# Optimization experiments

Hardware: AMD Instinct MI355X
Metric: run time of the kernel (lower is better)

Reference implementation:

```python
import jax, jax.numpy as jnp
import numpy as np

N_CLASS = 4432          # 1108 siRNA classes x 4 cell types
N_GROUPS = 4
GROUP_SIZE = N_CLASS // N_GROUPS  # 1108
LABEL_SMOOTHING = 0.1
CONFIDENCE = 1.0 - LABEL_SMOOTHING
SMOOTHING_VALUE = LABEL_SMOOTHING / (GROUP_SIZE - 1)


def setup_inputs() -> dict:
    key = jax.random.key(0)
    k1, k2 = jax.random.split(key)
    output = jax.random.normal(k1, (16384, N_CLASS), dtype=jnp.float32)
    target = jax.random.randint(k2, (16384,), 0, N_CLASS, dtype=jnp.int64)
    return {"output": output, "target": target}


def reference(output, target):
    # output: [B, C] logits, target: [B] int labels
    log_output = jax.nn.log_softmax(output, axis=1)                      # [B, C]
    classes = jnp.arange(N_CLASS, dtype=target.dtype)                    # [C]
    one_hot = jnp.where(classes[None, :] == target[:, None],
                        CONFIDENCE, SMOOTHING_VALUE).astype(output.dtype)  # [B, C]
    # group of each class (4 cell-type groups, contiguous blocks of GROUP_SIZE)
    class_group = classes // GROUP_SIZE                                  # [C]
    target_group = target // GROUP_SIZE                                  # [B]
    # zero smoothed mass for classes outside the sample's group (masks[group])
    one_hot = jnp.where(class_group[None, :] == target_group[:, None], one_hot, 0.0)
    loss = -(one_hot * log_output).sum(axis=1)                           # [B]
    return jnp.mean(loss)
```

## Files before the change

### kernel.cpp

```cpp
#include <hip/hip_runtime.h>
#include <math.h>

#define N_CLASS   4432
#define GROUP_SZ  1108
#define NV4       (N_CLASS / 4)
#define GV4       (GROUP_SZ / 4)
#define NROWS     16384
#define BLOCK     256

static constexpr float CONF   = 0.9f;
static constexpr float SMOOTH = 0.1f / (GROUP_SZ - 1);

template <bool WS_MODE>
__global__ __launch_bounds__(BLOCK)
void lsl_kernel(const float* __restrict__ logits,
                const int*   __restrict__ target,
                float*       __restrict__ sink) {
    const int row = blockIdx.x;
    const float4* __restrict__ rp = (const float4*)(logits + (size_t)row * N_CLASS);

    const int t      = target[row];
    const int g      = t / GROUP_SZ;
    const int glo    = g * GV4;
    const int ghi    = glo + GV4;
    const int tchunk = t >> 2;
    const int tlane  = t & 3;
    const int tid    = threadIdx.x;

    const int  c4    = tid + 1024;
    const bool have5 = (c4 < NV4);

    float4 v0 = rp[tid];
    float4 v1 = rp[tid + 256];
    float4 v2 = rp[tid + 512];
    float4 v3 = rp[tid + 768];
    float4 v4 = make_float4(-INFINITY, -INFINITY, -INFINITY, -INFINITY);
    if (have5) v4 = rp[c4];

    float m = fmaxf(fmaxf(fmaxf(v0.x, v0.y), fmaxf(v0.z, v0.w)),
                    fmaxf(fmaxf(v1.x, v1.y), fmaxf(v1.z, v1.w)));
    m = fmaxf(m, fmaxf(fmaxf(v2.x, v2.y), fmaxf(v2.z, v2.w)));
    m = fmaxf(m, fmaxf(fmaxf(v3.x, v3.y), fmaxf(v3.z, v3.w)));
    m = fmaxf(m, fmaxf(fmaxf(v4.x, v4.y), fmaxf(v4.z, v4.w)));

    #pragma unroll
    for (int off = 32; off > 0; off >>= 1)
        m = fmaxf(m, __shfl_xor(m, off));

    __shared__ float m_s[4], s_s[4], g_s[4];
    __shared__ float xt_s;
    const int wave = tid >> 6;
    const int lane = tid & 63;
    if (lane == 0) m_s[wave] = m;
    __syncthreads();
    const float M = fmaxf(fmaxf(m_s[0], m_s[1]), fmaxf(m_s[2], m_s[3]));

    float s = __expf(v0.x - M) + __expf(v0.y - M) + __expf(v0.z - M) + __expf(v0.w - M)
            + __expf(v1.x - M) + __expf(v1.y - M) + __expf(v1.z - M) + __expf(v1.w - M)
            + __expf(v2.x - M) + __expf(v2.y - M) + __expf(v2.z - M) + __expf(v2.w - M)
            + __expf(v3.x - M) + __expf(v3.y - M) + __expf(v3.z - M) + __expf(v3.w - M)
            + __expf(v4.x - M) + __expf(v4.y - M) + __expf(v4.z - M) + __expf(v4.w - M);

    float gsum = 0.f;
    {
        int c0 = tid;
        if (c0 >= glo && c0 < ghi) gsum += (v0.x + v0.y) + (v0.z + v0.w);
        int c1 = tid + 256;
        if (c1 >= glo && c1 < ghi) gsum += (v1.x + v1.y) + (v1.z + v1.w);
        int c2 = tid + 512;
        if (c2 >= glo && c2 < ghi) gsum += (v2.x + v2.y) + (v2.z + v2.w);
        int c3 = tid + 768;
        if (c3 >= glo && c3 < ghi) gsum += (v3.x + v3.y) + (v3.z + v3.w);
        if (have5 && c4 >= glo && c4 < ghi) gsum += (v4.x + v4.y) + (v4.z + v4.w);
    }

    {
        float4 tv; bool has_t = false;
        if (tid == tchunk)              { tv = v0; has_t = true; }
        else if (tid + 256 == tchunk)   { tv = v1; has_t = true; }
        else if (tid + 512 == tchunk)   { tv = v2; has_t = true; }
        else if (tid + 768 == tchunk)   { tv = v3; has_t = true; }
        else if (have5 && c4 == tchunk) { tv = v4; has_t = true; }
        if (has_t) {
            xt_s = (tlane == 0) ? tv.x : (tlane == 1) ? tv.y
                 : (tlane == 2) ? tv.z : tv.w;
        }
    }

    #pragma unroll
    for (int off = 32; off > 0; off >>= 1) {
        s    += __shfl_xor(s, off);
        gsum += __shfl_xor(gsum, off);
    }
    if (lane == 0) { s_s[wave] = s; g_s[wave] = gsum; }
    __syncthreads();

    if (tid == 0) {
        float S = (s_s[0] + s_s[1]) + (s_s[2] + s_s[3]);
        float G = (g_s[0] + g_s[1]) + (g_s[2] + g_s[3]);
        float lse  = M + __logf(S);
        float loss = lse - ((CONF - SMOOTH) * xt_s + SMOOTH * G);
        if (WS_MODE) sink[row] = loss;
        else         atomicAdd(sink, loss * (1.0f / NROWS));
    }
}

__global__ __launch_bounds__(256)
void lsl_reduce(const float* __restrict__ ws, float* __restrict__ out) {
    const float4* wp = (const float4*)ws;
    const int tid = threadIdx.x;
    float s = 0.f;
    #pragma unroll
    for (int i = 0; i < NROWS / 4 / 256; ++i) {
        float4 v = wp[tid + i * 256];
        s += (v.x + v.y) + (v.z + v.w);
    }
    #pragma unroll
    for (int off = 32; off > 0; off >>= 1) s += __shfl_xor(s, off);
    __shared__ float ss[4];
    const int wave = tid >> 6, lane = tid & 63;
    if (lane == 0) ss[wave] = s;
    __syncthreads();
    if (tid == 0) out[0] = ((ss[0] + ss[1]) + (ss[2] + ss[3])) * (1.0f / NROWS);
}

extern "C" void kernel_launch(void* const* d_in, const int* in_sizes, int n_in,
                              void* d_out, int out_size, void* d_ws, size_t ws_size,
                              hipStream_t stream) {
    const float* logits = (const float*)d_in[0];
    const int*   target = (const int*)d_in[1];
    float*       result = (float*)d_out;
    float*       ws     = (float*)d_ws;

    if (ws_size >= (size_t)NROWS * sizeof(float)) {
        lsl_kernel<true><<<NROWS, BLOCK, 0, stream>>>(logits, target, ws);
        lsl_reduce<<<1, 256, 0, stream>>>(ws, result);
    } else {
        hipMemsetAsync(result, 0, sizeof(float), stream);
        lsl_kernel<false><<<NROWS, BLOCK, 0, stream>>>(logits, target, result);
    }
}
```

Baseline: 381.9 us.

## Assign one wavefront per row and drop block-level syncs

Each 256-thread block now handles four rows, one per wavefront. Each lane loads 18 float4 chunks and all reductions (max, sum-exp, group sum, target logit) use wave shuffles only. This removes the shared-memory exchanges and the two __syncthreads per row, and gives each wave more outstanding loads. The cost is a larger register array per thread, which may reduce occupancy.

```diff
diff --git a/kernel.cpp b/kernel.cpp
--- a/kernel.cpp
+++ b/kernel.cpp
@@ -7,6 +7,9 @@
 #define GV4       (GROUP_SZ / 4)
 #define NROWS     16384
 #define BLOCK     256
+#define FULL_IT   17
+#define TAIL_BASE (FULL_IT * 64)
+#define TAIL_N    (NV4 - TAIL_BASE)
 
 static constexpr float CONF   = 0.9f;
 static constexpr float SMOOTH = 0.1f / (GROUP_SZ - 1);
@@ -16,7 +19,9 @@
 void lsl_kernel(const float* __restrict__ logits,
                 const int*   __restrict__ target,
                 float*       __restrict__ sink) {
-    const int row = blockIdx.x;
+    const int wave = threadIdx.x >> 6;
+    const int lane = threadIdx.x & 63;
+    const int row  = blockIdx.x * 4 + wave;
     const float4* __restrict__ rp = (const float4*)(logits + (size_t)row * N_CLASS);
 
     const int t      = target[row];
@@ -25,81 +30,50 @@
     const int ghi    = glo + GV4;
     const int tchunk = t >> 2;
     const int tlane  = t & 3;
-    const int tid    = threadIdx.x;
 
-    const int  c4    = tid + 1024;
-    const bool have5 = (c4 < NV4);
+    float4 v[FULL_IT + 1];
+    #pragma unroll
+    for (int i = 0; i < FULL_IT; ++i) v[i] = rp[lane + 64 * i];
+    const bool have18 = (lane < TAIL_N);
+    v[FULL_IT] = make_float4(-INFINITY, -INFINITY, -INFINITY, -INFINITY);
+    if (have18) v[FULL_IT] = rp[TAIL_BASE + lane];
 
-    float4 v0 = rp[tid];
-    float4 v1 = rp[tid + 256];
-    float4 v2 = rp[tid + 512];
-    float4 v3 = rp[tid + 768];
-    float4 v4 = make_float4(-INFINITY, -INFINITY, -INFINITY, -INFINITY);
-    if (have5) v4 = rp[c4];
-
-    float m = fmaxf(fmaxf(fmaxf(v0.x, v0.y), fmaxf(v0.z, v0.w)),
-                    fmaxf(fmaxf(v1.x, v1.y), fmaxf(v1.z, v1.w)));
-    m = fmaxf(m, fmaxf(fmaxf(v2.x, v2.y), fmaxf(v2.z, v2.w)));
-    m = fmaxf(m, fmaxf(fmaxf(v3.x, v3.y), fmaxf(v3.z, v3.w)));
-    m = fmaxf(m, fmaxf(fmaxf(v4.x, v4.y), fmaxf(v4.z, v4.w)));
-
+    float m = -INFINITY;
+    #pragma unroll
+    for (int i = 0; i <= FULL_IT; ++i)
+        m = fmaxf(m, fmaxf(fmaxf(v[i].x, v[i].y), fmaxf(v[i].z, v[i].w)));
     #pragma unroll
     for (int off = 32; off > 0; off >>= 1)
         m = fmaxf(m, __shfl_xor(m, off));
 
-    __shared__ float m_s[4], s_s[4], g_s[4];
-    __shared__ float xt_s;
-    const int wave = tid >> 6;
-    const int lane = tid & 63;
-    if (lane == 0) m_s[wave] = m;
-    __syncthreads();
-    const float M = fmaxf(fmaxf(m_s[0], m_s[1]), fmaxf(m_s[2], m_s[3]));
-
-    float s = __expf(v0.x - M) + __expf(v0.y - M) + __expf(v0.z - M) + __expf(v0.w - M)
-            + __expf(v1.x - M) + __expf(v1.y - M) + __expf(v1.z - M) + __expf(v1.w - M)
-            + __expf(v2.x - M) + __expf(v2.y - M) + __expf(v2.z - M) + __expf(v2.w - M)
-            + __expf(v3.x - M) + __expf(v3.y - M) + __expf(v3.z - M) + __expf(v3.w - M)
-            + __expf(v4.x - M) + __expf(v4.y - M) + __expf(v4.z - M) + __expf(v4.w - M);
-
-    float gsum = 0.f;
-    {
-        int c0 = tid;
-        if (c0 >= glo && c0 < ghi) gsum += (v0.x + v0.y) + (v0.z + v0.w);
-        int c1 = tid + 256;
-        if (c1 >= glo && c1 < ghi) gsum += (v1.x + v1.y) + (v1.z + v1.w);
-        int c2 = tid + 512;
-        if (c2 >= glo && c2 < ghi) gsum += (v2.x + v2.y) + (v2.z + v2.w);
-        int c3 = tid + 768;
-        if (c3 >= glo && c3 < ghi) gsum += (v3.x + v3.y) + (v3.z + v3.w);
-        if (have5 && c4 >= glo && c4 < ghi) gsum += (v4.x + v4.y) + (v4.z + v4.w);
+    float s = 0.f;
+    #pragma unroll
+    for (int i = 0; i <= FULL_IT; ++i) {
+        s += __expf(v[i].x - m) + __expf(v[i].y - m)
+           + __expf(v[i].z - m) + __expf(v[i].w - m);
     }
 
-    {
-        float4 tv; bool has_t = false;
-        if (tid == tchunk)              { tv = v0; has_t = true; }
-        else if (tid + 256 == tchunk)   { tv = v1; has_t = true; }
-        else if (tid + 512 == tchunk)   { tv = v2; has_t = true; }
-        else if (tid + 768 == tchunk)   { tv = v3; has_t = true; }
-        else if (have5 && c4 == tchunk) { tv = v4; has_t = true; }
-        if (has_t) {
-            xt_s = (tlane == 0) ? tv.x : (tlane == 1) ? tv.y
-                 : (tlane == 2) ? tv.z : tv.w;
-        }
+    float gsum = 0.f, xt = 0.f;
+    #pragma unroll
+    for (int i = 0; i <= FULL_IT; ++i) {
+        const int  c     = (i < FULL_IT) ? (lane + 64 * i) : (TAIL_BASE + lane);
+        const bool valid = (i < FULL_IT) || have18;
+        if (valid && c >= glo && c < ghi)
+            gsum += (v[i].x + v[i].y) + (v[i].z + v[i].w);
+        if (valid && c == tchunk)
+            xt = (tlane == 0) ? v[i].x : (tlane == 1) ? v[i].y
+               : (tlane == 2) ? v[i].z : v[i].w;
     }
 
     #pragma unroll
     for (int off = 32; off > 0; off >>= 1) {
         s    += __shfl_xor(s, off);
         gsum += __shfl_xor(gsum, off);
+        xt   += __shfl_xor(xt, off);
     }
-    if (lane == 0) { s_s[wave] = s; g_s[wave] = gsum; }
-    __syncthreads();
 
-    if (tid == 0) {
-        float S = (s_s[0] + s_s[1]) + (s_s[2] + s_s[3]);
-        float G = (g_s[0] + g_s[1]) + (g_s[2] + g_s[3]);
-        float lse  = M + __logf(S);
-        float loss = lse - ((CONF - SMOOTH) * xt_s + SMOOTH * G);
+    if (lane == 0) {
+        const float loss = (m + __logf(s)) - ((CONF - SMOOTH) * xt + SMOOTH * gsum);
         if (WS_MODE) sink[row] = loss;
         else         atomicAdd(sink, loss * (1.0f / NROWS));
     }
@@ -133,10 +107,10 @@
     float*       ws     = (float*)d_ws;
 
     if (ws_size >= (size_t)NROWS * sizeof(float)) {
-        lsl_kernel<true><<<NROWS, BLOCK, 0, stream>>>(logits, target, ws);
+        lsl_kernel<true><<<NROWS / 4, BLOCK, 0, stream>>>(logits, target, ws);
         lsl_reduce<<<1, 256, 0, stream>>>(ws, result);
     } else {
         hipMemsetAsync(result, 0, sizeof(float), stream);
-        lsl_kernel<false><<<NROWS, BLOCK, 0, stream>>>(logits, target, result);
+        lsl_kernel<false><<<NROWS / 4, BLOCK, 0, stream>>>(logits, target, result);
     }
 }
```

After: 381.8 us. About the same (-0.0%).
